# Kernel optimization log

Measured on AMD Instinct MI355X. Metric: run time of the kernel, lower is better.

The kernel has to match this reference:

```python
import jax, jax.numpy as jnp
import numpy as np

C = 384
K = 13
EPS = 1e-5

def bn(y, g, b, m, v):
    # inference-mode BatchNorm2d over channel dim of NCHW
    scale = (g / jnp.sqrt(v + EPS)).reshape(1, -1, 1, 1)
    shift = (b - m * g / jnp.sqrt(v + EPS)).reshape(1, -1, 1, 1)
    return y * scale + shift

def dwconv(x, w):
    # depthwise KxK conv, SAME padding, w: [C,1,K,K]
    p = w.shape[-1] // 2
    return jax.lax.conv_general_dilated(
        x, w, window_strides=(1, 1), padding=[(p, p), (p, p)],
        dimension_numbers=('NCHW', 'OIHW', 'NCHW'),
        feature_group_count=x.shape[1])

def setup_inputs() -> dict:
    key = jax.random.key(0)
    ks = jax.random.split(key, 16)
    f32 = jnp.float32
    inp = {
        'x':     jax.random.normal(ks[0], (16, C, 56, 56), dtype=f32),
        'pw_w':  jax.random.normal(ks[1], (C, C), dtype=f32) * 0.05,
        'pw_g':  jax.random.uniform(ks[2], (C,), dtype=f32) + 0.5,
        'pw_b':  jax.random.normal(ks[3], (C,), dtype=f32) * 0.1,
        'pw_m':  jax.random.normal(ks[4], (C,), dtype=f32) * 0.1,
        'pw_v':  jax.random.uniform(ks[5], (C,), dtype=f32) + 0.5,
        'dwk_w': jax.random.normal(ks[6], (C, 1, K, K), dtype=f32) * 0.05,
        'dwk_g': jax.random.uniform(ks[7], (C,), dtype=f32) + 0.5,
        'dwk_b': jax.random.normal(ks[8], (C,), dtype=f32) * 0.1,
        'dwk_m': jax.random.normal(ks[9], (C,), dtype=f32) * 0.1,
        'dwk_v': jax.random.uniform(ks[10], (C,), dtype=f32) + 0.5,
        'dw1_w': jax.random.normal(ks[11], (C,), dtype=f32) * 0.5,
        'dw1_g': jax.random.uniform(ks[12], (C,), dtype=f32) + 0.5,
        'dw1_b': jax.random.normal(ks[13], (C,), dtype=f32) * 0.1,
        'dw1_m': jax.random.normal(ks[14], (C,), dtype=f32) * 0.1,
        'dw1_v': jax.random.uniform(ks[15], (C,), dtype=f32) + 0.5,
    }
    return inp

def reference(x, pw_w, pw_g, pw_b, pw_m, pw_v,
              dwk_w, dwk_g, dwk_b, dwk_m, dwk_v,
              dw1_w, dw1_g, dw1_b, dw1_m, dw1_v):
    # pointwise conv (1x1, dense over channels) + BN, residual add
    y = jnp.einsum('bchw,oc->bohw', x, pw_w)
    x_pw = bn(y, pw_g, pw_b, pw_m, pw_v) + x
    # large-kernel depthwise branch
    out = bn(dwconv(x_pw, dwk_w), dwk_g, dwk_b, dwk_m, dwk_v)
    # 1x1 depthwise branch = per-channel scale
    out = out + bn(x_pw * dw1_w.reshape(1, -1, 1, 1), dw1_g, dw1_b, dw1_m, dw1_v)
    return jax.nn.gelu(out, approximate=False)
```

## Files before the change

kernel.cpp:

```cpp
#include <hip/hip_runtime.h>

#define CC 384
#define HW 3136
#define WIDTH 56
#define PLANE_ELEMS (CC*HW)
#define EPS 1e-5f

#define SLOT_U 6272
#define HALF_U 3136

#define WROW 40
#define WSTEP_U (CC*WROW)
#define WP_TOTAL (12*WSTEP_U)

typedef __attribute__((ext_vector_type(8))) short bf16x8;
typedef __attribute__((ext_vector_type(4))) float f32x4;

static __device__ __forceinline__ float bf2f(unsigned short u) {
  union { unsigned int i; float f; } x; x.i = ((unsigned int)u) << 16; return x.f;
}
static __device__ __forceinline__ unsigned short f2bf(float f) {
  union { float f; unsigned int i; } x; x.f = f;
  unsigned int r = x.i + 0x7fffu + ((x.i >> 16) & 1u);
  return (unsigned short)(r >> 16);
}

__global__ __launch_bounds__(256) void pack_w(
    const float* __restrict__ wmat, unsigned short* __restrict__ wp)
{
  int i = blockIdx.x * 256 + threadIdx.x;
  int kt  = i / WSTEP_U;
  int rem = i - kt * WSTEP_U;
  int o   = rem / WROW;
  int kk  = rem - o * WROW;
  unsigned short v = 0;
  if (kk < 32) v = f2bf(wmat[o * CC + kt * 32 + kk]);
  wp[i] = v;
}

__global__ __launch_bounds__(256, 3) void pw_gemm_bn_res(
    const float* __restrict__ xin,
    const unsigned short* __restrict__ wp,
    const float* __restrict__ pwg, const float* __restrict__ pwb,
    const float* __restrict__ pwm, const float* __restrict__ pwv,
    unsigned short* __restrict__ xpw)
{
  __shared__ __align__(16) unsigned short Xt[64 * 40];
  __shared__ __align__(16) unsigned short Wt[WSTEP_U];
  __shared__ float scaleS[CC];
  __shared__ float shiftS[CC];

  const int tid = threadIdx.x;
  const int j0 = blockIdx.x * 64;
  const int b  = blockIdx.y;
  const size_t bbase = (size_t)b * PLANE_ELEMS;

  for (int o = tid; o < CC; o += 256) {
    float s = pwg[o] * rsqrtf(pwv[o] + EPS);
    scaleS[o] = s;
    shiftS[o] = pwb[o] - pwm[o] * s;
  }

  const int lane = tid & 63;
  const int wid  = tid >> 6;
  const int l15  = lane & 15;
  const int q    = lane >> 4;

  f32x4 acc[4][6] = {};

  const float* xsrc0 = xin + bbase + (size_t)(wid * 8) * HW + (j0 + lane);

  for (int kt = 0; kt < 12; ++kt) {
    const int c0 = kt * 32;
    __syncthreads();
    {
      const float* src = xsrc0 + (size_t)c0 * HW;
      float v0 = src[0 * HW], v1 = src[1 * HW], v2 = src[2 * HW], v3 = src[3 * HW];
      float v4 = src[4 * HW], v5 = src[5 * HW], v6 = src[6 * HW], v7 = src[7 * HW];
      bf16x8 u;
      u[0] = (short)f2bf(v0); u[1] = (short)f2bf(v1);
      u[2] = (short)f2bf(v2); u[3] = (short)f2bf(v3);
      u[4] = (short)f2bf(v4); u[5] = (short)f2bf(v5);
      u[6] = (short)f2bf(v6); u[7] = (short)f2bf(v7);
      *((bf16x8*)&Xt[lane * 40 + wid * 8]) = u;
    }
    {
      const unsigned short* g = wp + (size_t)kt * WSTEP_U;
      #pragma unroll
      for (int i = 0; i < 8; ++i) {
        int c = i * 4 + wid;
        if (c < 30) {
          __builtin_amdgcn_global_load_lds(
              (const __attribute__((address_space(1))) unsigned int*)(g + c * 512 + lane * 8),
              (__attribute__((address_space(3))) unsigned int*)(&Wt[c * 512]),
              16, 0, 0);
        }
      }
    }
    __syncthreads();

    bf16x8 a[4];
    #pragma unroll
    for (int jf = 0; jf < 4; ++jf)
      a[jf] = *((const bf16x8*)&Xt[(jf * 16 + l15) * 40 + q * 8]);

    #pragma unroll
    for (int of = 0; of < 6; ++of) {
      bf16x8 bb = *((const bf16x8*)&Wt[(wid * 96 + of * 16 + l15) * WROW + q * 8]);
      #pragma unroll
      for (int jf = 0; jf < 4; ++jf)
        acc[jf][of] = __builtin_amdgcn_mfma_f32_16x16x32_bf16(a[jf], bb, acc[jf][of], 0, 0, 0);
    }
  }

  const int ob = wid * 96;
  #pragma unroll
  for (int of = 0; of < 6; ++of) {
    const int o = ob + of * 16 + l15;
    const float s = scaleS[o], t = shiftS[o];
    #pragma unroll
    for (int jf = 0; jf < 4; ++jf) {
      const int j = j0 + jf * 16 + q * 4;
      f32x4 av = acc[jf][of];
      float4 xr = *((const float4*)(xin + bbase + (size_t)o * HW + j));
      ushort4 w4;
      w4.x = f2bf(av[0] * s + t + xr.x);
      w4.y = f2bf(av[1] * s + t + xr.y);
      w4.z = f2bf(av[2] * s + t + xr.z);
      w4.w = f2bf(av[3] * s + t + xr.w);
      size_t pidx = (size_t)(b * CC + o) * SLOT_U + HALF_U + j;
      *((ushort4*)(xpw + pidx)) = w4;
    }
  }
}

#define TSTRIDE 88
#define TROWS 76

__global__ __launch_bounds__(256) void dw_conv_mfma(
    float* __restrict__ outf,
    const unsigned short* __restrict__ stash,
    const float* __restrict__ dwkw,
    const float* __restrict__ dkg, const float* __restrict__ dkb,
    const float* __restrict__ dkm, const float* __restrict__ dkv,
    const float* __restrict__ d1w,
    const float* __restrict__ d1g, const float* __restrict__ d1b,
    const float* __restrict__ d1m, const float* __restrict__ d1v)
{
  __shared__ __align__(16) unsigned short tile[TROWS * TSTRIDE];
  __shared__ __align__(16) unsigned short Bt[13 * 16 * 32];

  const int bc = blockIdx.x;
  const int c = bc % CC;
  const size_t plane_u = (size_t)bc * SLOT_U + HALF_U;
  const size_t plane_f = (size_t)bc * HW;
  const int tid = threadIdx.x;

  for (int i = tid; i < TROWS * TSTRIDE; i += 256) {
    int r = i / TSTRIDE, col = i - r * TSTRIDE;
    int gy = r - 6, gx = col - 6;
    unsigned short v = 0;
    if ((unsigned)gy < (unsigned)WIDTH && (unsigned)gx < (unsigned)WIDTH)
      v = stash[plane_u + gy * WIDTH + gx];
    tile[i] = v;
  }
  for (int i = tid; i < 13 * 512; i += 256) {
    int ky = i >> 9, rem = i & 511, n = rem >> 5, k = rem & 31;
    int kx = k - n;
    float wv = ((unsigned)kx < 13u) ? dwkw[c * 169 + ky * 13 + kx] : 0.f;
    Bt[i] = f2bf(wv);
  }

  const float sk = dkg[c] * rsqrtf(dkv[c] + EPS);
  const float tk = dkb[c] - dkm[c] * sk;
  const float s1 = d1g[c] * rsqrtf(d1v[c] + EPS);
  const float a1 = d1w[c] * s1;
  const float t1 = d1b[c] - d1m[c] * s1;
  const float tsum = tk + t1;

  __syncthreads();

  const int lane = tid & 63;
  const int l15  = lane & 15;
  const int q    = lane >> 4;
  const int wid  = tid >> 6;

  bf16x8 bfr[13];
  #pragma unroll
  for (int ky = 0; ky < 13; ++ky)
    bfr[ky] = *((const bf16x8*)&Bt[(ky * 16 + l15) * 32 + q * 8]);

  for (int t = wid; t < 16; t += 4) {
    const int y0 = (t >> 2) * 16, x0 = (t & 3) * 16;
    f32x4 acc = {0.f, 0.f, 0.f, 0.f};
    #pragma unroll
    for (int ky = 0; ky < 13; ++ky) {
      bf16x8 a = *((const bf16x8*)&tile[(y0 + l15 + ky) * TSTRIDE + x0 + q * 8]);
      acc = __builtin_amdgcn_mfma_f32_16x16x32_bf16(a, bfr[ky], acc, 0, 0, 0);
    }
    const int x = x0 + l15;
    if (x < WIDTH) {
      #pragma unroll
      for (int r = 0; r < 4; ++r) {
        const int y = y0 + q * 4 + r;
        if (y < WIDTH) {
          float ctr = bf2f(tile[(y + 6) * TSTRIDE + x + 6]);
          float v = acc[r] * sk + tsum + ctr * a1;
          outf[plane_f + y * WIDTH + x] =
              0.5f * v * (1.f + erff(v * 0.70710678118654752f));
        }
      }
    }
  }
}

extern "C" void kernel_launch(void* const* d_in, const int* in_sizes, int n_in,
                              void* d_out, int out_size, void* d_ws, size_t ws_size,
                              hipStream_t stream) {
  const float* x     = (const float*)d_in[0];
  const float* pw_w  = (const float*)d_in[1];
  const float* pw_g  = (const float*)d_in[2];
  const float* pw_b  = (const float*)d_in[3];
  const float* pw_m  = (const float*)d_in[4];
  const float* pw_v  = (const float*)d_in[5];
  const float* dwk_w = (const float*)d_in[6];
  const float* dwk_g = (const float*)d_in[7];
  const float* dwk_b = (const float*)d_in[8];
  const float* dwk_m = (const float*)d_in[9];
  const float* dwk_v = (const float*)d_in[10];
  const float* dw1_w = (const float*)d_in[11];
  const float* dw1_g = (const float*)d_in[12];
  const float* dw1_b = (const float*)d_in[13];
  const float* dw1_m = (const float*)d_in[14];
  const float* dw1_v = (const float*)d_in[15];
  float* outf = (float*)d_out;
  unsigned short* outu = (unsigned short*)d_out;
  unsigned short* wpack = (unsigned short*)d_ws;

  pack_w<<<WP_TOTAL / 256, 256, 0, stream>>>(pw_w, wpack);

  dim3 gridA(HW / 64, 16);
  pw_gemm_bn_res<<<gridA, 256, 0, stream>>>(x, wpack, pw_g, pw_b, pw_m, pw_v, outu);

  dim3 gridB(16 * CC);
  dw_conv_mfma<<<gridB, 256, 0, stream>>>(outf, outu, dwk_w,
      dwk_g, dwk_b, dwk_m, dwk_v, dw1_w, dw1_g, dw1_b, dw1_m, dw1_v);
}
```

Before: 291.7 us.

## Vectorize depthwise tile load and prepack banded conv weights via async LDS copy

The depthwise conv kernel now fills its input halo tile with 16-byte bf16x8 loads, shifting the tile by two columns to keep the loads aligned, and adjusts the weight band offset and centre tap to match. A new pack_bt kernel builds the banded bf16 weight matrix once per channel in workspace, and each conv block copies it straight into LDS with global_load_lds instead of recomputing it from fp32 weights in every block. This removes scalar 2-byte gathers and repeated per-block weight conversion, at the cost of an extra launch and a workspace-size check with a fallback path.

```diff
diff --git a/kernel.cpp b/kernel.cpp
--- a/kernel.cpp
+++ b/kernel.cpp
@@ -12,6 +12,9 @@
 #define WROW 40
 #define WSTEP_U (CC*WROW)
 #define WP_TOTAL (12*WSTEP_U)
+
+#define BT_U 6656
+#define BT_TOTAL (CC*BT_U)
 
 typedef __attribute__((ext_vector_type(8))) short bf16x8;
 typedef __attribute__((ext_vector_type(4))) float f32x4;
@@ -36,6 +39,19 @@
   unsigned short v = 0;
   if (kk < 32) v = f2bf(wmat[o * CC + kt * 32 + kk]);
   wp[i] = v;
+}
+
+__global__ __launch_bounds__(256) void pack_bt(
+    const float* __restrict__ dwkw, unsigned short* __restrict__ btg)
+{
+  const int c = blockIdx.x;
+  for (int i = threadIdx.x; i < BT_U; i += 256) {
+    int ky = i >> 9, rem = i & 511, n = rem >> 5, k = rem & 31;
+    int kx = k - n - 2;
+    unsigned short v = 0;
+    if ((unsigned)kx < 13u) v = f2bf(dwkw[c * 169 + ky * 13 + kx]);
+    btg[(size_t)c * BT_U + i] = v;
+  }
 }
 
 __global__ __launch_bounds__(256, 3) void pw_gemm_bn_res(
@@ -136,10 +152,12 @@
 
 #define TSTRIDE 88
 #define TROWS 76
+#define NCH 11
 
 __global__ __launch_bounds__(256) void dw_conv_mfma(
     float* __restrict__ outf,
     const unsigned short* __restrict__ stash,
+    const unsigned short* __restrict__ btg,
     const float* __restrict__ dwkw,
     const float* __restrict__ dkg, const float* __restrict__ dkb,
     const float* __restrict__ dkm, const float* __restrict__ dkv,
@@ -155,20 +173,37 @@
   const size_t plane_u = (size_t)bc * SLOT_U + HALF_U;
   const size_t plane_f = (size_t)bc * HW;
   const int tid = threadIdx.x;
-
-  for (int i = tid; i < TROWS * TSTRIDE; i += 256) {
-    int r = i / TSTRIDE, col = i - r * TSTRIDE;
-    int gy = r - 6, gx = col - 6;
-    unsigned short v = 0;
-    if ((unsigned)gy < (unsigned)WIDTH && (unsigned)gx < (unsigned)WIDTH)
-      v = stash[plane_u + gy * WIDTH + gx];
-    tile[i] = v;
-  }
-  for (int i = tid; i < 13 * 512; i += 256) {
-    int ky = i >> 9, rem = i & 511, n = rem >> 5, k = rem & 31;
-    int kx = k - n;
-    float wv = ((unsigned)kx < 13u) ? dwkw[c * 169 + ky * 13 + kx] : 0.f;
-    Bt[i] = f2bf(wv);
+  const int lane = tid & 63;
+  const int wid  = tid >> 6;
+
+  for (int i = tid; i < TROWS * NCH; i += 256) {
+    int r = i / NCH, ch = i - r * NCH;
+    int gy = r - 6;
+    bf16x8 v = {0,0,0,0,0,0,0,0};
+    if ((unsigned)gy < (unsigned)WIDTH && ch >= 1 && ch <= 7)
+      v = *((const bf16x8*)(stash + plane_u + gy * WIDTH + (ch - 1) * 8));
+    *((bf16x8*)&tile[r * TSTRIDE + ch * 8]) = v;
+  }
+
+  if (btg) {
+    const unsigned short* g = btg + (size_t)c * BT_U;
+    #pragma unroll
+    for (int i = 0; i < 4; ++i) {
+      int ch = i * 4 + wid;
+      if (ch < 13) {
+        __builtin_amdgcn_global_load_lds(
+            (const __attribute__((address_space(1))) unsigned int*)(g + ch * 512 + lane * 8),
+            (__attribute__((address_space(3))) unsigned int*)(&Bt[ch * 512]),
+            16, 0, 0);
+      }
+    }
+  } else {
+    for (int i = tid; i < 13 * 512; i += 256) {
+      int ky = i >> 9, rem = i & 511, n = rem >> 5, k = rem & 31;
+      int kx = k - n - 2;
+      float wv = ((unsigned)kx < 13u) ? dwkw[c * 169 + ky * 13 + kx] : 0.f;
+      Bt[i] = f2bf(wv);
+    }
   }
 
   const float sk = dkg[c] * rsqrtf(dkv[c] + EPS);
@@ -180,10 +215,8 @@
 
   __syncthreads();
 
-  const int lane = tid & 63;
   const int l15  = lane & 15;
   const int q    = lane >> 4;
-  const int wid  = tid >> 6;
 
   bf16x8 bfr[13];
   #pragma unroll
@@ -204,7 +237,7 @@
       for (int r = 0; r < 4; ++r) {
         const int y = y0 + q * 4 + r;
         if (y < WIDTH) {
-          float ctr = bf2f(tile[(y + 6) * TSTRIDE + x + 6]);
+          float ctr = bf2f(tile[(y + 6) * TSTRIDE + x + 8]);
           float v = acc[r] * sk + tsum + ctr * a1;
           outf[plane_f + y * WIDTH + x] =
               0.5f * v * (1.f + erff(v * 0.70710678118654752f));
@@ -239,10 +272,16 @@
 
   pack_w<<<WP_TOTAL / 256, 256, 0, stream>>>(pw_w, wpack);
 
+  unsigned short* btg = nullptr;
+  if (ws_size >= (size_t)(WP_TOTAL + BT_TOTAL) * sizeof(unsigned short)) {
+    btg = wpack + WP_TOTAL;
+    pack_bt<<<CC, 256, 0, stream>>>(dwk_w, btg);
+  }
+
   dim3 gridA(HW / 64, 16);
   pw_gemm_bn_res<<<gridA, 256, 0, stream>>>(x, wpack, pw_g, pw_b, pw_m, pw_v, outu);
 
   dim3 gridB(16 * CC);
-  dw_conv_mfma<<<gridB, 256, 0, stream>>>(outf, outu, dwk_w,
+  dw_conv_mfma<<<gridB, 256, 0, stream>>>(outf, outu, btg, dwk_w,
       dwk_g, dwk_b, dwk_m, dwk_v, dw1_w, dw1_g, dw1_b, dw1_m, dw1_v);
 }
```

Measured after the change: 255.4 us. -12.5%, faster.
